# Performance work log

Hardware: AMD Instinct MI355X
Metric: run time of the kernel (lower is better)

Reference implementation:

```python
import jax, jax.numpy as jnp
import numpy as np

REGION_SIZE = 3
BANDWIDTH = 0.5


def _extract_patches(x, R):
    # x: [B, C, H, W] -> patches [B, H', W', N, C], N = R*R, H' = H-R+1
    B, C, H, W = x.shape
    Hp, Wp = H - R + 1, W - R + 1
    shifts = [x[:, :, di:di + Hp, dj:dj + Wp] for di in range(R) for dj in range(R)]
    p = jnp.stack(shifts, axis=2)            # [B, C, N, H', W']
    return jnp.transpose(p, (0, 3, 4, 2, 1))  # [B, H', W', N, C]


def setup_inputs() -> dict:
    key = jax.random.key(0)
    x = jax.random.uniform(key, (4, 3, 256, 256), dtype=jnp.float32)
    return {"x": x}


def reference(x):
    R = REGION_SIZE
    h = jnp.asarray(BANDWIDTH, dtype=x.dtype)
    C = x.shape[1]
    N = R * R
    patches = _extract_patches(x, R)                      # [B,H',W',N,C]
    sq = jnp.sum(patches * patches, axis=-1)              # [B,H',W',N]
    gram = jnp.einsum('bhwnc,bhwmc->bhwnm', patches, patches)
    d2 = jnp.maximum(sq[..., :, None] + sq[..., None, :] - 2.0 * gram, 0.0)
    logits = -d2 / (2.0 * h * h)                          # [B,H',W',N,N]
    # log p_i = logsumexp_j logits_ij - log N - C*log(sqrt(2*pi)*h)
    log_norm = jnp.log(jnp.asarray(N, x.dtype)) + C * jnp.log(jnp.sqrt(2.0 * jnp.pi) * h)
    logp = jax.scipy.special.logsumexp(logits, axis=-1) - log_norm  # [B,H',W',N]
    return -jnp.mean(logp, axis=-1)                        # [B,H',W']
```

## Files before the change

### kernel.cpp

```cpp
#include <hip/hip_runtime.h>
#include <math.h>


#define TX 64
#define TY 4
#define HH 256
#define WW 256
#define HP 254
#define WP 254

__global__ __launch_bounds__(256) void je_kernel(const float* __restrict__ x,
                                                 float* __restrict__ out) {
    __shared__ float lds[3][TY + 2][TX + 2];

    const int b   = blockIdx.z;
    const int by  = blockIdx.y;
    const int bx  = blockIdx.x;
    const int tid = threadIdx.x;

    const int row0 = by * TY;
    const int col0 = bx * TX;

    const float* xb = x + (size_t)b * 3 * HH * WW;

    constexpr int NE = 3 * (TY + 2) * (TX + 2);
    for (int e = tid; e < NE; e += 256) {
        int c    = e / ((TY + 2) * (TX + 2));
        int rem  = e - c * ((TY + 2) * (TX + 2));
        int r    = rem / (TX + 2);
        int col  = rem - r * (TX + 2);
        int grow = row0 + r, gcol = col0 + col;
        float v = 0.0f;
        if (grow < HH && gcol < WW)
            v = xb[(size_t)c * HH * WW + (size_t)grow * WW + gcol];
        lds[c][r][col] = v;
    }
    __syncthreads();

    const int tx = tid & (TX - 1);
    const int ty = tid >> 6;
    const int i = row0 + ty, j = col0 + tx;
    if (i >= HP || j >= WP) return;

    float p[9][3];
#pragma unroll
    for (int c = 0; c < 3; ++c)
#pragma unroll
        for (int di = 0; di < 3; ++di)
#pragma unroll
            for (int dj = 0; dj < 3; ++dj)
                p[di * 3 + dj][c] = lds[c][ty + di][tx + dj];

    float s[9];
#pragma unroll
    for (int n = 0; n < 9; ++n) s[n] = 1.0f;

    const float K = -2.8853900818f;
#pragma unroll
    for (int n = 0; n < 9; ++n) {
#pragma unroll
        for (int m = n + 1; m < 9; ++m) {
            float d0 = p[n][0] - p[m][0];
            float d1 = p[n][1] - p[m][1];
            float d2 = p[n][2] - p[m][2];
            float dd = fmaf(d0, d0, fmaf(d1, d1, d2 * d2));
            float e = exp2f(dd * K);
            s[n] += e;
            s[m] += e;
        }
    }

    float acc = 0.0f;
#pragma unroll
    for (int n = 0; n < 9; ++n) acc += __log2f(s[n]);

    const float cst = 2.8745986353f;
    out[(size_t)b * HP * WP + (size_t)i * WP + j] = cst - acc * (0.69314718056f / 9.0f);
}

extern "C" void kernel_launch(void* const* d_in, const int* in_sizes, int n_in,
                              void* d_out, int out_size, void* d_ws, size_t ws_size,
                              hipStream_t stream) {
    const float* x = (const float*)d_in[0];
    float* out = (float*)d_out;

    dim3 grid((WP + TX - 1) / TX, (HP + TY - 1) / TY, 4);
    je_kernel<<<grid, 256, 0, stream>>>(x, out);
}
```

Measured before the change: 11.87 us.

## Compute four output pixels per thread from registers, dropping LDS staging

Removes the shared-memory tile and __syncthreads; each thread now loads its 3x6x3 input window straight from global memory with float4/float2 vector loads and computes four adjacent outputs, then writes them with float2 stores. The goal is less LDS traffic and per-pixel load overhead, plus fewer blocks through a flat 1D grid. The cost is higher register pressure, roughly 4x fewer threads (about 65K), and possible misaligned float2 stores, since the output row stride of 254 makes odd rows only 8-byte aligned.

Measured after the change: 10.49 us. 11.7% less time.

```diff
diff --git a/kernel.cpp b/kernel.cpp
--- a/kernel.cpp
+++ b/kernel.cpp
@@ -2,80 +2,81 @@
 #include <math.h>
 
 
-#define TX 64
-#define TY 4
-#define HH 256
-#define WW 256
 #define HP 254
 #define WP 254
 
 __global__ __launch_bounds__(256) void je_kernel(const float* __restrict__ x,
                                                  float* __restrict__ out) {
-    __shared__ float lds[3][TY + 2][TX + 2];
+    int t = blockIdx.x * 256 + threadIdx.x;
+    const int g = t & 63;
+    int rest = t >> 6;
+    const int i = rest % HP;
+    const int b = rest / HP;
+    const int j0 = g << 2;
 
-    const int b   = blockIdx.z;
-    const int by  = blockIdx.y;
-    const int bx  = blockIdx.x;
-    const int tid = threadIdx.x;
+    const float* xb = x + (size_t)b * 3 * 65536;
 
-    const int row0 = by * TY;
-    const int col0 = bx * TX;
+    float p[3][6][3];
+#pragma unroll
+    for (int c = 0; c < 3; ++c) {
+#pragma unroll
+        for (int r = 0; r < 3; ++r) {
+            const float* rowp = xb + c * 65536 + (i + r) * 256 + j0;
+            float4 v = *(const float4*)rowp;
+            p[r][0][c] = v.x; p[r][1][c] = v.y; p[r][2][c] = v.z; p[r][3][c] = v.w;
+            if (g < 63) {
+                float2 w = *(const float2*)(rowp + 4);
+                p[r][4][c] = w.x; p[r][5][c] = w.y;
+            } else {
+                p[r][4][c] = 0.0f; p[r][5][c] = 0.0f;
+            }
+        }
+    }
 
-    const float* xb = x + (size_t)b * 3 * HH * WW;
-
-    constexpr int NE = 3 * (TY + 2) * (TX + 2);
-    for (int e = tid; e < NE; e += 256) {
-        int c    = e / ((TY + 2) * (TX + 2));
-        int rem  = e - c * ((TY + 2) * (TX + 2));
-        int r    = rem / (TX + 2);
-        int col  = rem - r * (TX + 2);
-        int grow = row0 + r, gcol = col0 + col;
-        float v = 0.0f;
-        if (grow < HH && gcol < WW)
-            v = xb[(size_t)c * HH * WW + (size_t)grow * WW + gcol];
-        lds[c][r][col] = v;
-    }
-    __syncthreads();
-
-    const int tx = tid & (TX - 1);
-    const int ty = tid >> 6;
-    const int i = row0 + ty, j = col0 + tx;
-    if (i >= HP || j >= WP) return;
-
-    float p[9][3];
+    float s[4][9];
 #pragma unroll
-    for (int c = 0; c < 3; ++c)
+    for (int k = 0; k < 4; ++k)
 #pragma unroll
-        for (int di = 0; di < 3; ++di)
-#pragma unroll
-            for (int dj = 0; dj < 3; ++dj)
-                p[di * 3 + dj][c] = lds[c][ty + di][tx + dj];
-
-    float s[9];
-#pragma unroll
-    for (int n = 0; n < 9; ++n) s[n] = 1.0f;
+        for (int n = 0; n < 9; ++n) s[k][n] = 1.0f;
 
     const float K = -2.8853900818f;
 #pragma unroll
-    for (int n = 0; n < 9; ++n) {
+    for (int k = 0; k < 4; ++k) {
 #pragma unroll
-        for (int m = n + 1; m < 9; ++m) {
-            float d0 = p[n][0] - p[m][0];
-            float d1 = p[n][1] - p[m][1];
-            float d2 = p[n][2] - p[m][2];
-            float dd = fmaf(d0, d0, fmaf(d1, d1, d2 * d2));
-            float e = exp2f(dd * K);
-            s[n] += e;
-            s[m] += e;
+        for (int n = 0; n < 9; ++n) {
+            const int r1 = n / 3, c1 = k + n % 3;
+#pragma unroll
+            for (int m = n + 1; m < 9; ++m) {
+                const int r2 = m / 3, c2 = k + m % 3;
+                float d0 = p[r1][c1][0] - p[r2][c2][0];
+                float d1 = p[r1][c1][1] - p[r2][c2][1];
+                float d2 = p[r1][c1][2] - p[r2][c2][2];
+                float dd = fmaf(d0, d0, fmaf(d1, d1, d2 * d2));
+                float e = exp2f(dd * K);
+                s[k][n] += e;
+                s[k][m] += e;
+            }
         }
     }
 
-    float acc = 0.0f;
+    const float cst = 2.8745986353f;
+    float r0[4];
 #pragma unroll
-    for (int n = 0; n < 9; ++n) acc += __log2f(s[n]);
+    for (int k = 0; k < 4; ++k) {
+        float acc = 0.0f;
+#pragma unroll
+        for (int n = 0; n < 9; ++n) acc += __log2f(s[k][n]);
+        r0[k] = cst - acc * (0.69314718056f / 9.0f);
+    }
 
-    const float cst = 2.8745986353f;
-    out[(size_t)b * HP * WP + (size_t)i * WP + j] = cst - acc * (0.69314718056f / 9.0f);
+    float* op = out + (size_t)b * HP * WP + (size_t)i * WP + j0;
+    if (g < 63) {
+        *(float2*)op       = make_float2(r0[0], r0[1]);
+        *(float2*)(op + 2) = make_float2(r0[2], r0[3]);
+    } else {
+        op[0] = r0[0];
+        op[1] = r0[1];
+    }
 }
 
 extern "C" void kernel_launch(void* const* d_in, const int* in_sizes, int n_in,
@@ -83,7 +84,5 @@
                               hipStream_t stream) {
     const float* x = (const float*)d_in[0];
     float* out = (float*)d_out;
-
-    dim3 grid((WP + TX - 1) / TX, (HP + TY - 1) / TY, 4);
-    je_kernel<<<grid, 256, 0, stream>>>(x, out);
+    je_kernel<<<254, 256, 0, stream>>>(x, out);
 }
```
